# Kernel tuning notes

Hardware: AMD Instinct MI355X
Metric: run time of the kernel (lower is better)

## Reference

```python
import jax, jax.numpy as jnp
import numpy as np

MARGIN = 1.0
N, D = 4096, 512
NUM_CLASSES = 64


def setup_inputs() -> dict:
    key = jax.random.key(0)
    k1, k2 = jax.random.split(key)
    inputs = jax.random.normal(k1, (N, D), dtype=jnp.float32)
    targets = jax.random.randint(k2, (N,), 0, NUM_CLASSES, dtype=jnp.int64)
    return {"inputs": inputs, "targets": targets}


def reference(inputs, targets):
    n = inputs.shape[0]
    sq = jnp.sum(inputs * inputs, axis=1)  # [n]
    # squared Euclidean distances, clamped at 0 (matches relu in original)
    d2 = jnp.maximum(sq[:, None] + sq[None, :] - 2.0 * (inputs @ inputs.T), 0.0)
    # safe sqrt (zero entries get 0, matching forward; avoids NaN grads)
    dist = jnp.where(d2 > 0, jnp.sqrt(jnp.where(d2 > 0, d2, 1.0)), 0.0)  # [n,n]

    same = targets[:, None] == targets[None, :]
    eye = jnp.eye(n, dtype=bool)
    pos_mask = same & ~eye          # positives, diagonal excluded
    neg_mask = ~same                # negatives (diagonal is same-label, excluded)

    # per-row sum_k exp(margin - d_ik) over negatives  (replaces per-pair loop)
    neg_sum = jnp.sum(jnp.where(neg_mask, jnp.exp(MARGIN - dist), 0.0), axis=1)  # [n]

    # J_ij = log(neg_sum_i + neg_sum_j) + d_ij for positive pairs
    J = jnp.log(neg_sum[:, None] + neg_sum[None, :]) + dist
    triu_pos = jnp.triu(pos_mask)   # loop iterated over upper-triangular positives
    hinge2 = jnp.where(triu_pos, jax.nn.relu(J) ** 2, 0.0)

    # original divides by count of ALL positive entries (both triangles)
    len_p = jnp.sum(pos_mask).astype(jnp.float32)
    return jnp.sum(hinge2) / len_p
```

## Files before the change

kernel.cpp:

```cpp
#include <hip/hip_runtime.h>
#include <math.h>

#define NN 4096
#define DD 512
#define MARGINF 1.0f
#define NCLS 64
#define MAXM 160
#define TRI (MAXM * (MAXM - 1) / 2)

typedef __attribute__((ext_vector_type(8))) short bf16x8;
typedef __attribute__((ext_vector_type(4))) float f32x4;

#define WS_SQ   0
#define WS_NS   4096
#define WS_LOSS 8192
#define WS_CNT  8256
#define WS_RK   8320
#define WS_MEM  12416
#define WS_XB   32768
#define WS_PD   1081344

__device__ __forceinline__ unsigned short f2bf(float f) {
    unsigned u = __float_as_uint(f);
    u += 0x7fffu + ((u >> 16) & 1u);
    return (unsigned short)(u >> 16);
}

__device__ __forceinline__ void gl_lds16(const void* g, void* l) {
    __builtin_amdgcn_global_load_lds(
        (__attribute__((address_space(1))) unsigned int*)g,
        (__attribute__((address_space(3))) unsigned int*)l,
        16, 0, 0);
}

__global__ __launch_bounds__(256) void prep_kernel(const float* __restrict__ X,
                                                   float* __restrict__ ws) {
    const int wv = threadIdx.x >> 6, lane = threadIdx.x & 63;
    const int row = blockIdx.x * 4 + wv;
    const float4* xr = (const float4*)(X + (size_t)row * DD);
    float4 a = xr[lane], b = xr[lane + 64];
    float s = a.x * a.x + a.y * a.y + a.z * a.z + a.w * a.w
            + b.x * b.x + b.y * b.y + b.z * b.z + b.w * b.w;
#pragma unroll
    for (int off = 32; off; off >>= 1) s += __shfl_down(s, off, 64);
    if (lane == 0) { ws[WS_SQ + row] = s; ws[WS_NS + row] = 0.0f; }
    ushort4 pa = {f2bf(a.x), f2bf(a.y), f2bf(a.z), f2bf(a.w)};
    ushort4 pb = {f2bf(b.x), f2bf(b.y), f2bf(b.z), f2bf(b.w)};
    ushort4* xb = (ushort4*)((unsigned short*)(ws + WS_XB) + (size_t)row * DD);
    xb[lane] = pa;
    xb[lane + 64] = pb;
    if (blockIdx.x == 0) {
        if (threadIdx.x < NCLS) ((int*)(ws + WS_CNT))[threadIdx.x] = 0;
        if (threadIdx.x == 0) ws[WS_LOSS] = 0.0f;
    }
}

__global__ __launch_bounds__(256) void class_build_kernel(const int* __restrict__ tgt,
                                                          float* __restrict__ ws) {
    const int t = blockIdx.x * 256 + threadIdx.x;
    const int c = tgt[t];
    int* counts = (int*)(ws + WS_CNT);
    int* rk  = (int*)(ws + WS_RK);
    int* mem = (int*)(ws + WS_MEM);
    int p = atomicAdd(&counts[c], 1);
    rk[t] = p;
    if (p < MAXM) mem[c * MAXM + p] = t;
}

__global__ __launch_bounds__(256) void negsum_kernel(const int* __restrict__ tgt,
                                                     float* __restrict__ ws) {
    __shared__ unsigned short As[128 * 32];
    __shared__ unsigned short Bs[128 * 32];

    const int bidx = blockIdx.x;
    int bj = (int)((sqrtf(8.0f * (float)bidx + 1.0f) - 1.0f) * 0.5f);
    while (bj * (bj + 1) / 2 > bidx) --bj;
    while ((bj + 1) * (bj + 2) / 2 <= bidx) ++bj;
    const int bi = bidx - bj * (bj + 1) / 2;
    const int i0 = bi * 128, j0 = bj * 128;

    const int tid = threadIdx.x;
    const int w = tid >> 6, lane = tid & 63;
    const int lr = lane >> 2, lc = lane & 3;
    const unsigned short* Xb = (const unsigned short*)(ws + WS_XB);

    const unsigned short* ga0 = Xb + (size_t)(i0 + w * 16 + lr) * DD + lc * 8;
    const unsigned short* ga1 = ga0 + (size_t)64 * DD;
    const unsigned short* gb0 = Xb + (size_t)(j0 + w * 16 + lr) * DD + lc * 8;
    const unsigned short* gb1 = gb0 + (size_t)64 * DD;
    unsigned short* la0 = &As[(w * 16) * 32];
    unsigned short* la1 = &As[(64 + w * 16) * 32];
    unsigned short* lb0 = &Bs[(w * 16) * 32];
    unsigned short* lb1 = &Bs[(64 + w * 16) * 32];

    const int m_ = lane & 15, q = lane >> 4;
    const int wrow = (w >> 1) * 64, wcol = (w & 1) * 64;

    f32x4 acc[4][4] = {};

    for (int k0 = 0; k0 < DD; k0 += 32) {
        __syncthreads();
        gl_lds16(ga0 + k0, la0);
        gl_lds16(ga1 + k0, la1);
        gl_lds16(gb0 + k0, lb0);
        gl_lds16(gb1 + k0, lb1);
        __syncthreads();
        bf16x8 af[4], bf[4];
#pragma unroll
        for (int u = 0; u < 4; ++u)
            af[u] = *(const bf16x8*)&As[(wrow + u * 16 + m_) * 32 + q * 8];
#pragma unroll
        for (int v = 0; v < 4; ++v)
            bf[v] = *(const bf16x8*)&Bs[(wcol + v * 16 + m_) * 32 + q * 8];
#pragma unroll
        for (int u = 0; u < 4; ++u)
#pragma unroll
            for (int v = 0; v < 4; ++v)
                acc[u][v] = __builtin_amdgcn_mfma_f32_16x16x32_bf16(
                    af[u], bf[v], acc[u][v], 0, 0, 0);
    }

    const float* sq = ws + WS_SQ;
    float* ns = ws + WS_NS;
    const int* rk = (const int*)(ws + WS_RK);
    float* posd = ws + WS_PD;
    float sjv[4]; int tjv[4], jv[4];
#pragma unroll
    for (int v = 0; v < 4; ++v) {
        int j = j0 + wcol + v * 16 + m_;
        jv[v] = j;
        sjv[v] = sq[j];
        tjv[v] = tgt[j];
    }
    float colp[4] = {0.0f, 0.0f, 0.0f, 0.0f};
#pragma unroll
    for (int u = 0; u < 4; ++u) {
#pragma unroll
        for (int r = 0; r < 4; ++r) {
            const int i = i0 + wrow + u * 16 + q * 4 + r;
            const float si = sq[i];
            const int ti = tgt[i];
            float rp = 0.0f;
#pragma unroll
            for (int v = 0; v < 4; ++v) {
                float d2 = si + sjv[v] - 2.0f * acc[u][v][r];
                float dist = d2 > 0.0f ? sqrtf(d2) : 0.0f;
                if (tjv[v] != ti) {
                    float e = __expf(MARGINF - dist);
                    rp += e;
                    colp[v] += e;
                } else if (i < jv[v]) {
                    int ra = rk[i], rb = rk[jv[v]];
                    if (ra < MAXM && rb < MAXM) {
                        int hi = ra > rb ? ra : rb;
                        int lo = ra > rb ? rb : ra;
                        posd[ti * TRI + hi * (hi - 1) / 2 + lo] = dist;
                    }
                }
            }
            rp += __shfl_xor(rp, 1, 64);
            rp += __shfl_xor(rp, 2, 64);
            rp += __shfl_xor(rp, 4, 64);
            rp += __shfl_xor(rp, 8, 64);
            if (m_ == 0) atomicAdd(&ns[i], rp);
        }
    }
    if (bi != bj) {
#pragma unroll
        for (int v = 0; v < 4; ++v) {
            float cp = colp[v];
            cp += __shfl_xor(cp, 16, 64);
            cp += __shfl_xor(cp, 32, 64);
            if (q == 0) atomicAdd(&ns[jv[v]], cp);
        }
    }
}

__global__ __launch_bounds__(256) void pair2_kernel(float* __restrict__ ws) {
    __shared__ float wsum[4];
    const int c = blockIdx.x;
    int mc = ((const int*)(ws + WS_CNT))[c];
    if (mc > MAXM) mc = MAXM;
    const int P = mc * (mc - 1) / 2;
    const int* mem = (const int*)(ws + WS_MEM) + c * MAXM;
    const float* pd = ws + WS_PD + c * TRI;
    const float* ns = ws + WS_NS;
    float lsum = 0.0f;
    for (int p = threadIdx.x; p < P; p += 256) {
        int b = (int)((1.0f + sqrtf(1.0f + 8.0f * (float)p)) * 0.5f);
        while (b * (b - 1) / 2 > p) --b;
        while ((b + 1) * b / 2 <= p) ++b;
        const int a = p - b * (b - 1) / 2;
        const float dist = pd[b * (b - 1) / 2 + a];
        const int i = mem[a], j = mem[b];
        float J = __logf(ns[i] + ns[j]) + dist;
        float h = fmaxf(J, 0.0f);
        lsum += h * h;
    }
#pragma unroll
    for (int off = 32; off; off >>= 1) lsum += __shfl_xor(lsum, off, 64);
    const int wv = threadIdx.x >> 6, lane = threadIdx.x & 63;
    if (lane == 0) wsum[wv] = lsum;
    __syncthreads();
    if (threadIdx.x == 0) {
        float s = wsum[0] + wsum[1] + wsum[2] + wsum[3];
        if (s != 0.0f) atomicAdd(&ws[WS_LOSS], s);
    }
}

__global__ void finalize_kernel(const float* __restrict__ ws, float* __restrict__ out) {
    const int t = threadIdx.x;
    int mcv = (t < NCLS) ? ((const int*)(ws + WS_CNT))[t] : 0;
    float lp = (float)(mcv * (mcv - 1));
#pragma unroll
    for (int off = 32; off; off >>= 1) lp += __shfl_down(lp, off, 64);
    if (t == 0) out[0] = ws[WS_LOSS] / lp;
}

extern "C" void kernel_launch(void* const* d_in, const int* in_sizes, int n_in,
                              void* d_out, int out_size, void* d_ws, size_t ws_size,
                              hipStream_t stream) {
    const float* X  = (const float*)d_in[0];
    const int*  tgt = (const int*)d_in[1];
    float* ws  = (float*)d_ws;
    float* out = (float*)d_out;

    hipLaunchKernelGGL(prep_kernel, dim3(NN / 4), dim3(256), 0, stream, X, ws);
    hipLaunchKernelGGL(class_build_kernel, dim3(NN / 256), dim3(256), 0, stream, tgt, ws);
    hipLaunchKernelGGL(negsum_kernel, dim3(528), dim3(256), 0, stream, tgt, ws);
    hipLaunchKernelGGL(pair2_kernel, dim3(NCLS), dim3(256), 0, stream, ws);
    hipLaunchKernelGGL(finalize_kernel, dim3(1), dim3(64), 0, stream, ws, out);
}
```

Measured before the change: 121.7 us.

## Fuse class build into prep, double-buffer negsum GEMM, fold finalize into pair kernel

Class bucketing moves into prep_kernel, with one atomic per row. Workspace zeroing moves to a memset. The finalize step now runs in the last pair2 block, chosen by an atomic ticket counter. negsum_kernel uses 512 threads with double-buffered LDS tiles, so global-to-LDS loads for the next k-step overlap the MFMA work and each tile needs one barrier per iteration instead of two. The aim is fewer kernel launches and hidden load latency, at the cost of a memset node and a more complex last-block synchronization.

```diff
diff --git a/kernel.cpp b/kernel.cpp
--- a/kernel.cpp
+++ b/kernel.cpp
@@ -14,6 +14,7 @@
 #define WS_SQ   0
 #define WS_NS   4096
 #define WS_LOSS 8192
+#define WS_CTR  8193
 #define WS_CNT  8256
 #define WS_RK   8320
 #define WS_MEM  12416
@@ -34,6 +35,7 @@
 }
 
 __global__ __launch_bounds__(256) void prep_kernel(const float* __restrict__ X,
+                                                   const int* __restrict__ tgt,
                                                    float* __restrict__ ws) {
     const int wv = threadIdx.x >> 6, lane = threadIdx.x & 63;
     const int row = blockIdx.x * 4 + wv;
@@ -43,34 +45,24 @@
             + b.x * b.x + b.y * b.y + b.z * b.z + b.w * b.w;
 #pragma unroll
     for (int off = 32; off; off >>= 1) s += __shfl_down(s, off, 64);
-    if (lane == 0) { ws[WS_SQ + row] = s; ws[WS_NS + row] = 0.0f; }
+    if (lane == 0) {
+        ws[WS_SQ + row] = s;
+        int c = tgt[row];
+        int p = atomicAdd(&((int*)(ws + WS_CNT))[c], 1);
+        ((int*)(ws + WS_RK))[row] = p;
+        if (p < MAXM) ((int*)(ws + WS_MEM))[c * MAXM + p] = row;
+    }
     ushort4 pa = {f2bf(a.x), f2bf(a.y), f2bf(a.z), f2bf(a.w)};
     ushort4 pb = {f2bf(b.x), f2bf(b.y), f2bf(b.z), f2bf(b.w)};
     ushort4* xb = (ushort4*)((unsigned short*)(ws + WS_XB) + (size_t)row * DD);
     xb[lane] = pa;
     xb[lane + 64] = pb;
-    if (blockIdx.x == 0) {
-        if (threadIdx.x < NCLS) ((int*)(ws + WS_CNT))[threadIdx.x] = 0;
-        if (threadIdx.x == 0) ws[WS_LOSS] = 0.0f;
-    }
-}
-
-__global__ __launch_bounds__(256) void class_build_kernel(const int* __restrict__ tgt,
-                                                          float* __restrict__ ws) {
-    const int t = blockIdx.x * 256 + threadIdx.x;
-    const int c = tgt[t];
-    int* counts = (int*)(ws + WS_CNT);
-    int* rk  = (int*)(ws + WS_RK);
-    int* mem = (int*)(ws + WS_MEM);
-    int p = atomicAdd(&counts[c], 1);
-    rk[t] = p;
-    if (p < MAXM) mem[c * MAXM + p] = t;
-}
-
-__global__ __launch_bounds__(256) void negsum_kernel(const int* __restrict__ tgt,
-                                                     float* __restrict__ ws) {
-    __shared__ unsigned short As[128 * 32];
-    __shared__ unsigned short Bs[128 * 32];
+}
+
+__global__ __launch_bounds__(512, 2) void negsum_kernel(const int* __restrict__ tgt,
+                                                        float* __restrict__ ws) {
+    __shared__ unsigned short As[2][128 * 32];
+    __shared__ unsigned short Bs[2][128 * 32];
 
     const int bidx = blockIdx.x;
     int bj = (int)((sqrtf(8.0f * (float)bidx + 1.0f) - 1.0f) * 0.5f);
@@ -81,43 +73,40 @@
 
     const int tid = threadIdx.x;
     const int w = tid >> 6, lane = tid & 63;
-    const int lr = lane >> 2, lc = lane & 3;
     const unsigned short* Xb = (const unsigned short*)(ws + WS_XB);
 
-    const unsigned short* ga0 = Xb + (size_t)(i0 + w * 16 + lr) * DD + lc * 8;
-    const unsigned short* ga1 = ga0 + (size_t)64 * DD;
-    const unsigned short* gb0 = Xb + (size_t)(j0 + w * 16 + lr) * DD + lc * 8;
-    const unsigned short* gb1 = gb0 + (size_t)64 * DD;
-    unsigned short* la0 = &As[(w * 16) * 32];
-    unsigned short* la1 = &As[(64 + w * 16) * 32];
-    unsigned short* lb0 = &Bs[(w * 16) * 32];
-    unsigned short* lb1 = &Bs[(64 + w * 16) * 32];
+    const unsigned short* gA = Xb + (size_t)(i0 + w * 16 + (lane >> 2)) * DD + (lane & 3) * 8;
+    const unsigned short* gB = Xb + (size_t)(j0 + w * 16 + (lane >> 2)) * DD + (lane & 3) * 8;
 
     const int m_ = lane & 15, q = lane >> 4;
-    const int wrow = (w >> 1) * 64, wcol = (w & 1) * 64;
-
-    f32x4 acc[4][4] = {};
-
-    for (int k0 = 0; k0 < DD; k0 += 32) {
+    const int wr = (w & 3) * 32;
+    const int wc = (w >> 2) * 64;
+
+    f32x4 acc[2][4] = {};
+
+    gl_lds16(gA, As[0] + w * 512);
+    gl_lds16(gB, Bs[0] + w * 512);
+
+    for (int it = 0; it < 16; ++it) {
+        const int buf = it & 1;
         __syncthreads();
-        gl_lds16(ga0 + k0, la0);
-        gl_lds16(ga1 + k0, la1);
-        gl_lds16(gb0 + k0, lb0);
-        gl_lds16(gb1 + k0, lb1);
-        __syncthreads();
-        bf16x8 af[4], bf[4];
-#pragma unroll
-        for (int u = 0; u < 4; ++u)
-            af[u] = *(const bf16x8*)&As[(wrow + u * 16 + m_) * 32 + q * 8];
+        if (it + 1 < 16) {
+            gl_lds16(gA + (it + 1) * 32, As[buf ^ 1] + w * 512);
+            gl_lds16(gB + (it + 1) * 32, Bs[buf ^ 1] + w * 512);
+        }
+        bf16x8 af[2], bfr[4];
+#pragma unroll
+        for (int u = 0; u < 2; ++u)
+            af[u] = *(const bf16x8*)(As[buf] + (wr + u * 16 + m_) * 32 + q * 8);
 #pragma unroll
         for (int v = 0; v < 4; ++v)
-            bf[v] = *(const bf16x8*)&Bs[(wcol + v * 16 + m_) * 32 + q * 8];
-#pragma unroll
-        for (int u = 0; u < 4; ++u)
+            bfr[v] = *(const bf16x8*)(Bs[buf] + (wc + v * 16 + m_) * 32 + q * 8);
+#pragma unroll
+        for (int u = 0; u < 2; ++u)
 #pragma unroll
             for (int v = 0; v < 4; ++v)
                 acc[u][v] = __builtin_amdgcn_mfma_f32_16x16x32_bf16(
-                    af[u], bf[v], acc[u][v], 0, 0, 0);
+                    af[u], bfr[v], acc[u][v], 0, 0, 0);
     }
 
     const float* sq = ws + WS_SQ;
@@ -127,17 +116,17 @@
     float sjv[4]; int tjv[4], jv[4];
 #pragma unroll
     for (int v = 0; v < 4; ++v) {
-        int j = j0 + wcol + v * 16 + m_;
+        int j = j0 + wc + v * 16 + m_;
         jv[v] = j;
         sjv[v] = sq[j];
         tjv[v] = tgt[j];
     }
     float colp[4] = {0.0f, 0.0f, 0.0f, 0.0f};
 #pragma unroll
-    for (int u = 0; u < 4; ++u) {
+    for (int u = 0; u < 2; ++u) {
 #pragma unroll
         for (int r = 0; r < 4; ++r) {
-            const int i = i0 + wrow + u * 16 + q * 4 + r;
+            const int i = i0 + wr + u * 16 + q * 4 + r;
             const float si = sq[i];
             const int ti = tgt[i];
             float rp = 0.0f;
@@ -176,9 +165,12 @@
     }
 }
 
-__global__ __launch_bounds__(256) void pair2_kernel(float* __restrict__ ws) {
+__global__ __launch_bounds__(256) void pair2_kernel(float* __restrict__ ws,
+                                                    float* __restrict__ out) {
     __shared__ float wsum[4];
+    __shared__ bool last;
     const int c = blockIdx.x;
+    const int tid = threadIdx.x;
     int mc = ((const int*)(ws + WS_CNT))[c];
     if (mc > MAXM) mc = MAXM;
     const int P = mc * (mc - 1) / 2;
@@ -186,7 +178,7 @@
     const float* pd = ws + WS_PD + c * TRI;
     const float* ns = ws + WS_NS;
     float lsum = 0.0f;
-    for (int p = threadIdx.x; p < P; p += 256) {
+    for (int p = tid; p < P; p += 256) {
         int b = (int)((1.0f + sqrtf(1.0f + 8.0f * (float)p)) * 0.5f);
         while (b * (b - 1) / 2 > p) --b;
         while ((b + 1) * b / 2 <= p) ++b;
@@ -199,22 +191,27 @@
     }
 #pragma unroll
     for (int off = 32; off; off >>= 1) lsum += __shfl_xor(lsum, off, 64);
-    const int wv = threadIdx.x >> 6, lane = threadIdx.x & 63;
+    const int wv = tid >> 6, lane = tid & 63;
     if (lane == 0) wsum[wv] = lsum;
     __syncthreads();
-    if (threadIdx.x == 0) {
+    if (tid == 0) {
         float s = wsum[0] + wsum[1] + wsum[2] + wsum[3];
         if (s != 0.0f) atomicAdd(&ws[WS_LOSS], s);
-    }
-}
-
-__global__ void finalize_kernel(const float* __restrict__ ws, float* __restrict__ out) {
-    const int t = threadIdx.x;
-    int mcv = (t < NCLS) ? ((const int*)(ws + WS_CNT))[t] : 0;
-    float lp = (float)(mcv * (mcv - 1));
-#pragma unroll
-    for (int off = 32; off; off >>= 1) lp += __shfl_down(lp, off, 64);
-    if (t == 0) out[0] = ws[WS_LOSS] / lp;
+        __threadfence();
+        unsigned d = atomicAdd((unsigned*)&ws[WS_CTR], 1u);
+        last = (d == NCLS - 1);
+    }
+    __syncthreads();
+    if (last && tid < 64) {
+        int mcv = ((const int*)(ws + WS_CNT))[tid];
+        float lp = (float)(mcv * (mcv - 1));
+#pragma unroll
+        for (int off = 32; off; off >>= 1) lp += __shfl_down(lp, off, 64);
+        if (tid == 0) {
+            float total = atomicAdd(&ws[WS_LOSS], 0.0f);
+            out[0] = total / lp;
+        }
+    }
 }
 
 extern "C" void kernel_launch(void* const* d_in, const int* in_sizes, int n_in,
@@ -225,9 +222,8 @@
     float* ws  = (float*)d_ws;
     float* out = (float*)d_out;
 
-    hipLaunchKernelGGL(prep_kernel, dim3(NN / 4), dim3(256), 0, stream, X, ws);
-    hipLaunchKernelGGL(class_build_kernel, dim3(NN / 256), dim3(256), 0, stream, tgt, ws);
-    hipLaunchKernelGGL(negsum_kernel, dim3(528), dim3(256), 0, stream, tgt, ws);
-    hipLaunchKernelGGL(pair2_kernel, dim3(NCLS), dim3(256), 0, stream, ws);
-    hipLaunchKernelGGL(finalize_kernel, dim3(1), dim3(64), 0, stream, ws, out);
-}
+    hipMemsetAsync(ws + WS_NS, 0, (8320 - 4096) * sizeof(float), stream);
+    hipLaunchKernelGGL(prep_kernel, dim3(NN / 4), dim3(256), 0, stream, X, tgt, ws);
+    hipLaunchKernelGGL(negsum_kernel, dim3(528), dim3(512), 0, stream, tgt, ws);
+    hipLaunchKernelGGL(pair2_kernel, dim3(NCLS), dim3(256), 0, stream, ws, out);
+}
```

After: 136.6 us. 1.12x slower.
